# Performance work log

Measured on AMD Instinct MI355X. Metric: run time of the kernel, lower is better.

The kernel has to match this reference:

```python
import jax, jax.numpy as jnp
import numpy as np

B, T, C, H = 4, 4096, 1024, 64  # batch, seq, n_embd, head_size

def setup_inputs() -> dict:
    key = jax.random.key(0)
    kx, kq, kk, kv = jax.random.split(key, 4)
    x = jax.random.normal(kx, (B, T, C), dtype=jnp.float32)
    s = 1.0 / np.sqrt(C)
    Wq = jax.random.normal(kq, (C, H), dtype=jnp.float32) * s
    Wk = jax.random.normal(kk, (C, H), dtype=jnp.float32) * s
    Wv = jax.random.normal(kv, (C, H), dtype=jnp.float32) * s
    return {"x": x, "Wq": Wq, "Wk": Wk, "Wv": Wv}

def reference(x, Wq, Wk, Wv):
    B_, T_, C_ = x.shape
    q = x @ Wq  # [B,T,H]
    k = x @ Wk
    v = x @ Wv
    # NOTE: original scales by C**-0.5 (n_embd), not head_size**-0.5
    scale = jnp.asarray(C_, x.dtype) ** -0.5
    wei = jnp.einsum('bth,bsh->bts', q, k) * scale  # [B,T,T]
    causal = jnp.tril(jnp.ones((T_, T_), dtype=bool))
    wei = jnp.where(causal, wei, -jnp.inf)
    wei = jax.nn.softmax(wei, axis=-1)
    out = jnp.einsum('bts,bsh->bth', wei, v)  # [B,T,H]
    return out
```

## Files before the change

kernel.cpp:

```cpp
#include <hip/hip_runtime.h>
#include <hip/hip_bf16.h>
#include <math.h>

#define BB 4
#define TT 4096
#define CC 1024
#define HH 64

typedef __attribute__((ext_vector_type(8))) short short8;
typedef __attribute__((ext_vector_type(8))) unsigned short ushort8;
typedef __attribute__((ext_vector_type(4))) float f32x4;
typedef __attribute__((ext_vector_type(2))) unsigned int uint2v;

__device__ inline unsigned short f2bf(float f) {
    unsigned int u = __builtin_bit_cast(unsigned int, f);
    unsigned int r = u + 0x7fffu + ((u >> 16) & 1u);
    return (unsigned short)(r >> 16);
}

__device__ inline int soff_strip(int qs) {
    if (qs < 128) return (qs - 64) * 2;
    if (qs < 192) return 128 + (qs - 128) * 3;
    return 320 + (qs - 192) * 4;
}

__global__ __launch_bounds__(256) void wtrans_kernel(
    const float* __restrict__ Wq,
    const float* __restrict__ Wk,
    const float* __restrict__ Wv,
    unsigned short* __restrict__ Wf)
{
    const int t = blockIdx.x * 256 + threadIdx.x;
    const int lane = t & 63;
    const int ntl  = (t >> 6) % 12;
    const int kt   = t / 768;
    const int quad = lane >> 4, n = lane & 15;
    const int m    = ntl >> 2;
    const int col  = (ntl & 3) * 16 + n;
    const float* src = (m == 0) ? Wq : (m == 1) ? Wk : Wv;
    ushort8 u;
#pragma unroll
    for (int j = 0; j < 8; ++j)
        u[j] = f2bf(src[(kt * 32 + quad * 8 + j) * 64 + col]);
    *(ushort8*)(Wf + (size_t)t * 8) = u;
}

__global__ __launch_bounds__(256) void qkv_gemm(
    const float* __restrict__ x,
    const unsigned short* __restrict__ Wf,
    unsigned short* __restrict__ Qb,
    unsigned short* __restrict__ Kb,
    unsigned short* __restrict__ Vb)
{
    __shared__ f32x4 red[2][12][64];

    const int tid  = threadIdx.x;
    const int lane = tid & 63;
    const int wave = tid >> 6;
    const int n    = lane & 15;
    const int quad = lane >> 4;
    const int row0 = blockIdx.x * 16;

    const float* xp = x + (size_t)(row0 + n) * CC + wave * 256 + quad * 8;

    f32x4 acc[12];
#pragma unroll
    for (int i = 0; i < 12; ++i) acc[i] = (f32x4){0.f, 0.f, 0.f, 0.f};

#pragma unroll
    for (int kt = 0; kt < 8; ++kt) {
        const float4 f0 = *(const float4*)(xp + kt * 32);
        const float4 f1 = *(const float4*)(xp + kt * 32 + 4);
        short8 a;
        a[0] = (short)f2bf(f0.x); a[1] = (short)f2bf(f0.y);
        a[2] = (short)f2bf(f0.z); a[3] = (short)f2bf(f0.w);
        a[4] = (short)f2bf(f1.x); a[5] = (short)f2bf(f1.y);
        a[6] = (short)f2bf(f1.z); a[7] = (short)f2bf(f1.w);

        const unsigned short* wp = Wf + ((size_t)((wave * 8 + kt) * 12) * 64 + lane) * 8;
#pragma unroll
        for (int ntl = 0; ntl < 12; ++ntl) {
            const short8 bw = *(const short8*)(wp + (size_t)ntl * 64 * 8);
            acc[ntl] = __builtin_amdgcn_mfma_f32_16x16x32_bf16(a, bw, acc[ntl], 0, 0, 0);
        }
    }

    if (wave >= 2) {
#pragma unroll
        for (int ntl = 0; ntl < 12; ++ntl) red[wave - 2][ntl][lane] = acc[ntl];
    }
    __syncthreads();
    if (wave < 2) {
#pragma unroll
        for (int ntl = 0; ntl < 12; ++ntl) acc[ntl] += red[wave][ntl][lane];
    }
    __syncthreads();
    if (wave == 1) {
#pragma unroll
        for (int ntl = 0; ntl < 12; ++ntl) red[0][ntl][lane] = acc[ntl];
    }
    __syncthreads();
    if (wave == 0) {
#pragma unroll
        for (int ntl = 0; ntl < 12; ++ntl) {
            f32x4 s = acc[ntl] + red[0][ntl][lane];
            const int m    = ntl >> 2;
            const int colb = (ntl & 3) * 16;
            unsigned short* dst = (m == 0) ? Qb : (m == 1) ? Kb : Vb;
            const float sc = (m == 0) ? 0.03125f : 1.0f;
#pragma unroll
            for (int r = 0; r < 4; ++r) {
                const int row = row0 + quad * 4 + r;
                dst[(size_t)row * HH + colb + n] = f2bf(s[r] * sc);
            }
        }
    }
}

__global__ __launch_bounds__(256) void kv_repack(
    const unsigned short* __restrict__ Kb,
    const unsigned short* __restrict__ Vb,
    unsigned short* __restrict__ Kf,
    unsigned short* __restrict__ Vf)
{
    const int t = blockIdx.x * 256 + threadIdx.x;
    const int mat  = t >> 17;
    const int r    = t & 131071;
    const int lane = r & 63;
    const int kk   = (r >> 6) & 1;
    const int tile = (r >> 7) & 3;
    const int st   = (r >> 9) & 63;
    const int b    = r >> 15;
    const int n = lane & 15, quad = lane >> 4;

    if (mat == 0) {
        const unsigned short* src =
            Kb + ((size_t)b * TT + st * 64 + tile * 16 + n) * HH + kk * 32 + quad * 8;
        *(ushort8*)(Kf + (size_t)r * 8) = *(const ushort8*)src;
    } else {
        const int s0 = st * 64 + kk * 32 + quad * 8;
        const int h  = tile * 16 + n;
        ushort8 u;
#pragma unroll
        for (int j = 0; j < 8; ++j)
            u[j] = Vb[((size_t)b * TT + s0 + j) * HH + h];
        *(ushort8*)(Vf + (size_t)r * 8) = u;
    }
}

__global__ __launch_bounds__(256) void attn_kernel(
    const unsigned short* __restrict__ Qb,
    const unsigned short* __restrict__ Kf,
    const unsigned short* __restrict__ Vf,
    float* __restrict__ out,
    float* __restrict__ scr)
{
    __shared__ unsigned short Ps[4][16][72];

    const int tid  = threadIdx.x;
    const int lane = tid & 63;
    const int wave = tid >> 6;
    const int n    = lane & 15;
    const int quad = lane >> 4;

    const int wid = blockIdx.x * 4 + wave;
    const int b   = wid / 640;
    const int u   = wid - b * 640;

    int qs, ci;
    if (u < 64)        { qs = u;                  ci = 0; }
    else if (u < 192)  { const int v = u - 64;  qs = 64  + (v >> 1); ci = v & 1; }
    else if (u < 384)  { const int v = u - 192; const int d = v / 3;
                         qs = 128 + d;            ci = v - 3 * d; }
    else               { const int v = u - 384; qs = 192 + (v >> 2); ci = v & 3; }

    const int stmax = qs >> 2;
    const int st0   = ci << 4;
    const int stEnd = min(stmax, st0 + 15);
    const int nc    = (stmax + 16) >> 4;
    const int qrow  = qs * 16 + n;

    const unsigned short* qp = Qb + ((size_t)b * TT + qrow) * HH;
    const short8 bQ0 = *(const short8*)(qp + quad * 8);
    const short8 bQ1 = *(const short8*)(qp + 32 + quad * 8);

    const unsigned short* KfB = Kf + (size_t)b * 262144;
    const unsigned short* VfB = Vf + (size_t)b * 262144;

    f32x4 O[4];
#pragma unroll
    for (int ht = 0; ht < 4; ++ht) O[ht] = (f32x4){0.f, 0.f, 0.f, 0.f};
    float l = 0.f;

    for (int st = st0; st <= stEnd; ++st) {
        f32x4 S[4];
#pragma unroll
        for (int mt = 0; mt < 4; ++mt) {
            const unsigned short* kp = KfB + (size_t)((st * 4 + mt) * 2) * 512 + lane * 8;
            const short8 a0 = *(const short8*)(kp);
            const short8 a1 = *(const short8*)(kp + 512);
            f32x4 acc = (f32x4){0.f, 0.f, 0.f, 0.f};
            acc = __builtin_amdgcn_mfma_f32_16x16x32_bf16(a0, bQ0, acc, 0, 0, 0);
            acc = __builtin_amdgcn_mfma_f32_16x16x32_bf16(a1, bQ1, acc, 0, 0, 0);
            S[mt] = acc;
        }

        if (st == stmax) {
#pragma unroll
            for (int mt = 0; mt < 4; ++mt) {
                const int sg = st * 64 + mt * 16 + quad * 4;
#pragma unroll
                for (int r = 0; r < 4; ++r)
                    if (sg + r > qrow) S[mt][r] = -INFINITY;
            }
        }

#pragma unroll
        for (int mt = 0; mt < 4; ++mt)
#pragma unroll
            for (int r = 0; r < 4; ++r) {
                const float p = __expf(fminf(S[mt][r], 30.f));
                S[mt][r] = p;
                l += p;
            }

#pragma unroll
        for (int mt = 0; mt < 4; ++mt) {
            uint2v w;
            w[0] = (unsigned int)f2bf(S[mt][0]) | ((unsigned int)f2bf(S[mt][1]) << 16);
            w[1] = (unsigned int)f2bf(S[mt][2]) | ((unsigned int)f2bf(S[mt][3]) << 16);
            *(uint2v*)&Ps[wave][n][mt * 16 + quad * 4] = w;
        }
        asm volatile("s_waitcnt lgkmcnt(0)" ::: "memory");
        const short8 bP0 = *(const short8*)&Ps[wave][n][quad * 8];
        const short8 bP1 = *(const short8*)&Ps[wave][n][32 + quad * 8];

#pragma unroll
        for (int ht = 0; ht < 4; ++ht) {
            const unsigned short* vp = VfB + (size_t)((st * 4 + ht) * 2) * 512 + lane * 8;
            const short8 a0 = *(const short8*)(vp);
            const short8 a1 = *(const short8*)(vp + 512);
            O[ht] = __builtin_amdgcn_mfma_f32_16x16x32_bf16(a0, bP0, O[ht], 0, 0, 0);
            O[ht] = __builtin_amdgcn_mfma_f32_16x16x32_bf16(a1, bP1, O[ht], 0, 0, 0);
        }
    }

    l += __shfl_xor(l, 16);
    l += __shfl_xor(l, 32);

    if (nc == 1) {
        const float inv = 1.0f / l;
        float* op = out + ((size_t)b * TT + qrow) * HH;
#pragma unroll
        for (int ht = 0; ht < 4; ++ht) {
            float4 o4;
            o4.x = O[ht][0] * inv;
            o4.y = O[ht][1] * inv;
            o4.z = O[ht][2] * inv;
            o4.w = O[ht][3] * inv;
            *(float4*)(op + ht * 16 + quad * 4) = o4;
        }
    } else {
        float* sb = scr + (size_t)(b * 576 + soff_strip(qs) + ci) * 1040;
        float* rp = sb + n * 64;
#pragma unroll
        for (int ht = 0; ht < 4; ++ht)
            *(f32x4*)(rp + ht * 16 + quad * 4) = O[ht];
        if (quad == 0) sb[1024 + n] = l;
    }
}

__global__ __launch_bounds__(64) void combine_kernel(
    const float* __restrict__ scr,
    float* __restrict__ out)
{
    const int b  = blockIdx.x / 192;
    const int qs = 64 + blockIdx.x % 192;
    const int nc = ((qs >> 2) + 16) >> 4;
    const int base = b * 576 + soff_strip(qs);

    const int t    = threadIdx.x;
    const int row  = t >> 2;
    const int col0 = (t & 3) * 16;

    f32x4 s0 = (f32x4){0.f,0.f,0.f,0.f}, s1 = s0, s2 = s0, s3 = s0;
    float lsum = 0.f;
    for (int ci = 0; ci < nc; ++ci) {
        const float* sb = scr + (size_t)(base + ci) * 1040;
        lsum += sb[1024 + row];
        const float* p = sb + row * 64 + col0;
        s0 += *(const f32x4*)(p);
        s1 += *(const f32x4*)(p + 4);
        s2 += *(const f32x4*)(p + 8);
        s3 += *(const f32x4*)(p + 12);
    }
    const float inv = 1.0f / lsum;
    float* op = out + ((size_t)b * TT + qs * 16 + row) * HH + col0;
    *(f32x4*)(op)      = s0 * inv;
    *(f32x4*)(op + 4)  = s1 * inv;
    *(f32x4*)(op + 8)  = s2 * inv;
    *(f32x4*)(op + 12) = s3 * inv;
}

extern "C" void kernel_launch(void* const* d_in, const int* in_sizes, int n_in,
                              void* d_out, int out_size, void* d_ws, size_t ws_size,
                              hipStream_t stream)
{
    const float* x  = (const float*)d_in[0];
    const float* Wq = (const float*)d_in[1];
    const float* Wk = (const float*)d_in[2];
    const float* Wv = (const float*)d_in[3];

    unsigned short* Qb = (unsigned short*)d_ws;
    unsigned short* Kb = Qb + (size_t)BB * TT * HH;
    unsigned short* Vb = Kb + (size_t)BB * TT * HH;
    unsigned short* Wf = Vb + (size_t)BB * TT * HH;
    unsigned short* Kf = Wf + (size_t)192 * 1024;
    unsigned short* Vf = Kf + (size_t)BB * 262144;
    float*          scr = (float*)(Vf + (size_t)BB * 262144);
    float* out = (float*)d_out;

    wtrans_kernel<<<96, 256, 0, stream>>>(Wq, Wk, Wv, Wf);
    qkv_gemm<<<BB * TT / 16, 256, 0, stream>>>(x, Wf, Qb, Kb, Vb);
    kv_repack<<<1024, 256, 0, stream>>>(Kb, Vb, Kf, Vf);
    attn_kernel<<<640, 256, 0, stream>>>(Qb, Kf, Vf, out, scr);
    combine_kernel<<<768, 64, 0, stream>>>(scr, out);
}
```

Before: 160.0 us.

## Fuse K/V repack into QKV GEMM and prefetch K/V tiles in attention

The QKV projection now handles 32 rows per block, so each weight fragment feeds two MFMAs. It stages the fp32 results in shared memory and writes Q plus K and V directly in the fragment layouts the attention kernel reads, which removes the separate kv_repack kernel and the Kb/Vb round trip through global memory. The attention loop now software-prefetches the next K tile and issues the V loads before the softmax. It also double-buffers the P scratch in shared memory. The cost is more registers and 49KB of shared memory per GEMM block, which may reduce occupancy.

```diff
diff --git a/kernel.cpp b/kernel.cpp
--- a/kernel.cpp
+++ b/kernel.cpp
@@ -49,102 +49,125 @@
     const float* __restrict__ x,
     const unsigned short* __restrict__ Wf,
     unsigned short* __restrict__ Qb,
-    unsigned short* __restrict__ Kb,
-    unsigned short* __restrict__ Vb)
-{
-    __shared__ f32x4 red[2][12][64];
+    unsigned short* __restrict__ Kf,
+    unsigned short* __restrict__ Vf)
+{
+    __shared__ __align__(16) unsigned char smem[50176];
+    f32x4 (*red)[24][64] = (f32x4 (*)[24][64])smem;
+    float (*Tl)[200]     = (float (*)[200])(smem + 24576);
 
     const int tid  = threadIdx.x;
     const int lane = tid & 63;
     const int wave = tid >> 6;
     const int n    = lane & 15;
     const int quad = lane >> 4;
-    const int row0 = blockIdx.x * 16;
-
-    const float* xp = x + (size_t)(row0 + n) * CC + wave * 256 + quad * 8;
-
-    f32x4 acc[12];
-#pragma unroll
-    for (int i = 0; i < 12; ++i) acc[i] = (f32x4){0.f, 0.f, 0.f, 0.f};
+
+    const int row0g = blockIdx.x * 32;
+    const int b     = row0g >> 12;
+    const int trow  = row0g & (TT - 1);
+    const int st    = trow >> 6;
+    const int mtb   = (trow >> 4) & 3;
+    const int kkv   = (trow >> 5) & 1;
+
+    const float* xp0 = x + (size_t)(row0g + n) * CC + wave * 256 + quad * 8;
+    const float* xp1 = xp0 + 16 * CC;
+
+    f32x4 acc[2][12];
+#pragma unroll
+    for (int mtl = 0; mtl < 2; ++mtl)
+#pragma unroll
+        for (int i = 0; i < 12; ++i) acc[mtl][i] = (f32x4){0.f, 0.f, 0.f, 0.f};
 
 #pragma unroll
     for (int kt = 0; kt < 8; ++kt) {
-        const float4 f0 = *(const float4*)(xp + kt * 32);
-        const float4 f1 = *(const float4*)(xp + kt * 32 + 4);
-        short8 a;
-        a[0] = (short)f2bf(f0.x); a[1] = (short)f2bf(f0.y);
-        a[2] = (short)f2bf(f0.z); a[3] = (short)f2bf(f0.w);
-        a[4] = (short)f2bf(f1.x); a[5] = (short)f2bf(f1.y);
-        a[6] = (short)f2bf(f1.z); a[7] = (short)f2bf(f1.w);
+        const float4 f0 = *(const float4*)(xp0 + kt * 32);
+        const float4 f1 = *(const float4*)(xp0 + kt * 32 + 4);
+        const float4 g0 = *(const float4*)(xp1 + kt * 32);
+        const float4 g1 = *(const float4*)(xp1 + kt * 32 + 4);
+        short8 a0, a1;
+        a0[0] = (short)f2bf(f0.x); a0[1] = (short)f2bf(f0.y);
+        a0[2] = (short)f2bf(f0.z); a0[3] = (short)f2bf(f0.w);
+        a0[4] = (short)f2bf(f1.x); a0[5] = (short)f2bf(f1.y);
+        a0[6] = (short)f2bf(f1.z); a0[7] = (short)f2bf(f1.w);
+        a1[0] = (short)f2bf(g0.x); a1[1] = (short)f2bf(g0.y);
+        a1[2] = (short)f2bf(g0.z); a1[3] = (short)f2bf(g0.w);
+        a1[4] = (short)f2bf(g1.x); a1[5] = (short)f2bf(g1.y);
+        a1[6] = (short)f2bf(g1.z); a1[7] = (short)f2bf(g1.w);
 
         const unsigned short* wp = Wf + ((size_t)((wave * 8 + kt) * 12) * 64 + lane) * 8;
 #pragma unroll
         for (int ntl = 0; ntl < 12; ++ntl) {
             const short8 bw = *(const short8*)(wp + (size_t)ntl * 64 * 8);
-            acc[ntl] = __builtin_amdgcn_mfma_f32_16x16x32_bf16(a, bw, acc[ntl], 0, 0, 0);
+            acc[0][ntl] = __builtin_amdgcn_mfma_f32_16x16x32_bf16(a0, bw, acc[0][ntl], 0, 0, 0);
+            acc[1][ntl] = __builtin_amdgcn_mfma_f32_16x16x32_bf16(a1, bw, acc[1][ntl], 0, 0, 0);
         }
     }
 
     if (wave >= 2) {
 #pragma unroll
-        for (int ntl = 0; ntl < 12; ++ntl) red[wave - 2][ntl][lane] = acc[ntl];
+        for (int mtl = 0; mtl < 2; ++mtl)
+#pragma unroll
+            for (int ntl = 0; ntl < 12; ++ntl)
+                red[wave - 2][mtl * 12 + ntl][lane] = acc[mtl][ntl];
     }
     __syncthreads();
     if (wave < 2) {
 #pragma unroll
-        for (int ntl = 0; ntl < 12; ++ntl) acc[ntl] += red[wave][ntl][lane];
+        for (int mtl = 0; mtl < 2; ++mtl)
+#pragma unroll
+            for (int ntl = 0; ntl < 12; ++ntl)
+                acc[mtl][ntl] += red[wave][mtl * 12 + ntl][lane];
     }
     __syncthreads();
     if (wave == 1) {
 #pragma unroll
-        for (int ntl = 0; ntl < 12; ++ntl) red[0][ntl][lane] = acc[ntl];
+        for (int mtl = 0; mtl < 2; ++mtl)
+#pragma unroll
+            for (int ntl = 0; ntl < 12; ++ntl)
+                red[0][mtl * 12 + ntl][lane] = acc[mtl][ntl];
     }
     __syncthreads();
     if (wave == 0) {
 #pragma unroll
-        for (int ntl = 0; ntl < 12; ++ntl) {
-            f32x4 s = acc[ntl] + red[0][ntl][lane];
-            const int m    = ntl >> 2;
-            const int colb = (ntl & 3) * 16;
-            unsigned short* dst = (m == 0) ? Qb : (m == 1) ? Kb : Vb;
-            const float sc = (m == 0) ? 0.03125f : 1.0f;
-#pragma unroll
-            for (int r = 0; r < 4; ++r) {
-                const int row = row0 + quad * 4 + r;
-                dst[(size_t)row * HH + colb + n] = f2bf(s[r] * sc);
+        for (int mtl = 0; mtl < 2; ++mtl)
+#pragma unroll
+            for (int ntl = 0; ntl < 12; ++ntl) {
+                const f32x4 s = acc[mtl][ntl] + red[0][mtl * 12 + ntl][lane];
+                const int col = (ntl >> 2) * 64 + (ntl & 3) * 16 + n;
+#pragma unroll
+                for (int r = 0; r < 4; ++r)
+                    Tl[mtl * 16 + quad * 4 + r][col] = s[r];
             }
-        }
-    }
-}
-
-__global__ __launch_bounds__(256) void kv_repack(
-    const unsigned short* __restrict__ Kb,
-    const unsigned short* __restrict__ Vb,
-    unsigned short* __restrict__ Kf,
-    unsigned short* __restrict__ Vf)
-{
-    const int t = blockIdx.x * 256 + threadIdx.x;
-    const int mat  = t >> 17;
-    const int r    = t & 131071;
-    const int lane = r & 63;
-    const int kk   = (r >> 6) & 1;
-    const int tile = (r >> 7) & 3;
-    const int st   = (r >> 9) & 63;
-    const int b    = r >> 15;
-    const int n = lane & 15, quad = lane >> 4;
-
-    if (mat == 0) {
-        const unsigned short* src =
-            Kb + ((size_t)b * TT + st * 64 + tile * 16 + n) * HH + kk * 32 + quad * 8;
-        *(ushort8*)(Kf + (size_t)r * 8) = *(const ushort8*)src;
-    } else {
-        const int s0 = st * 64 + kk * 32 + quad * 8;
-        const int h  = tile * 16 + n;
+    }
+    __syncthreads();
+
+    {
+        const int row = tid & 31;
+        const int cq  = (tid >> 5) * 8;
         ushort8 u;
 #pragma unroll
         for (int j = 0; j < 8; ++j)
-            u[j] = Vb[((size_t)b * TT + s0 + j) * HH + h];
-        *(ushort8*)(Vf + (size_t)r * 8) = u;
+            u[j] = f2bf(Tl[row][cq + j] * 0.03125f);
+        *(ushort8*)(Qb + (size_t)(row0g + row) * HH + cq) = u;
+    }
+    {
+        const int mtl = wave & 1;
+        const int kk  = wave >> 1;
+        ushort8 u;
+#pragma unroll
+        for (int j = 0; j < 8; ++j)
+            u[j] = f2bf(Tl[mtl * 16 + n][64 + kk * 32 + quad * 8 + j]);
+        const size_t r = (size_t)(((b * 64 + st) * 4 + (mtb + mtl)) * 2 + kk) * 64 + lane;
+        *(ushort8*)(Kf + r * 8) = u;
+    }
+    {
+        const int ht = wave;
+        ushort8 u;
+#pragma unroll
+        for (int j = 0; j < 8; ++j)
+            u[j] = f2bf(Tl[quad * 8 + j][128 + ht * 16 + n]);
+        const size_t r = (size_t)(((b * 64 + st) * 4 + ht) * 2 + kkv) * 64 + lane;
+        *(ushort8*)(Vf + r * 8) = u;
     }
 }
 
@@ -155,7 +178,7 @@
     float* __restrict__ out,
     float* __restrict__ scr)
 {
-    __shared__ unsigned short Ps[4][16][72];
+    __shared__ unsigned short Ps[4][2][16][72];
 
     const int tid  = threadIdx.x;
     const int lane = tid & 63;
@@ -192,17 +215,38 @@
     for (int ht = 0; ht < 4; ++ht) O[ht] = (f32x4){0.f, 0.f, 0.f, 0.f};
     float l = 0.f;
 
+    short8 kA[4], kB[4];
+#pragma unroll
+    for (int mt = 0; mt < 4; ++mt) {
+        const unsigned short* kp = KfB + (size_t)((st0 * 4 + mt) * 2) * 512 + lane * 8;
+        kA[mt] = *(const short8*)(kp);
+        kB[mt] = *(const short8*)(kp + 512);
+    }
+
     for (int st = st0; st <= stEnd; ++st) {
         f32x4 S[4];
 #pragma unroll
         for (int mt = 0; mt < 4; ++mt) {
-            const unsigned short* kp = KfB + (size_t)((st * 4 + mt) * 2) * 512 + lane * 8;
-            const short8 a0 = *(const short8*)(kp);
-            const short8 a1 = *(const short8*)(kp + 512);
             f32x4 acc = (f32x4){0.f, 0.f, 0.f, 0.f};
-            acc = __builtin_amdgcn_mfma_f32_16x16x32_bf16(a0, bQ0, acc, 0, 0, 0);
-            acc = __builtin_amdgcn_mfma_f32_16x16x32_bf16(a1, bQ1, acc, 0, 0, 0);
+            acc = __builtin_amdgcn_mfma_f32_16x16x32_bf16(kA[mt], bQ0, acc, 0, 0, 0);
+            acc = __builtin_amdgcn_mfma_f32_16x16x32_bf16(kB[mt], bQ1, acc, 0, 0, 0);
             S[mt] = acc;
+        }
+
+        short8 vA[4], vB[4];
+#pragma unroll
+        for (int ht = 0; ht < 4; ++ht) {
+            const unsigned short* vp = VfB + (size_t)((st * 4 + ht) * 2) * 512 + lane * 8;
+            vA[ht] = *(const short8*)(vp);
+            vB[ht] = *(const short8*)(vp + 512);
+        }
+        if (st < stEnd) {
+#pragma unroll
+            for (int mt = 0; mt < 4; ++mt) {
+                const unsigned short* kp = KfB + (size_t)(((st + 1) * 4 + mt) * 2) * 512 + lane * 8;
+                kA[mt] = *(const short8*)(kp);
+                kB[mt] = *(const short8*)(kp + 512);
+            }
         }
 
         if (st == stmax) {
@@ -224,24 +268,22 @@
                 l += p;
             }
 
+        const int pp = st & 1;
 #pragma unroll
         for (int mt = 0; mt < 4; ++mt) {
             uint2v w;
             w[0] = (unsigned int)f2bf(S[mt][0]) | ((unsigned int)f2bf(S[mt][1]) << 16);
             w[1] = (unsigned int)f2bf(S[mt][2]) | ((unsigned int)f2bf(S[mt][3]) << 16);
-            *(uint2v*)&Ps[wave][n][mt * 16 + quad * 4] = w;
+            *(uint2v*)&Ps[wave][pp][n][mt * 16 + quad * 4] = w;
         }
         asm volatile("s_waitcnt lgkmcnt(0)" ::: "memory");
-        const short8 bP0 = *(const short8*)&Ps[wave][n][quad * 8];
-        const short8 bP1 = *(const short8*)&Ps[wave][n][32 + quad * 8];
+        const short8 bP0 = *(const short8*)&Ps[wave][pp][n][quad * 8];
+        const short8 bP1 = *(const short8*)&Ps[wave][pp][n][32 + quad * 8];
 
 #pragma unroll
         for (int ht = 0; ht < 4; ++ht) {
-            const unsigned short* vp = VfB + (size_t)((st * 4 + ht) * 2) * 512 + lane * 8;
-            const short8 a0 = *(const short8*)(vp);
-            const short8 a1 = *(const short8*)(vp + 512);
-            O[ht] = __builtin_amdgcn_mfma_f32_16x16x32_bf16(a0, bP0, O[ht], 0, 0, 0);
-            O[ht] = __builtin_amdgcn_mfma_f32_16x16x32_bf16(a1, bP1, O[ht], 0, 0, 0);
+            O[ht] = __builtin_amdgcn_mfma_f32_16x16x32_bf16(vA[ht], bP0, O[ht], 0, 0, 0);
+            O[ht] = __builtin_amdgcn_mfma_f32_16x16x32_bf16(vB[ht], bP1, O[ht], 0, 0, 0);
         }
     }
 
@@ -312,17 +354,14 @@
     const float* Wv = (const float*)d_in[3];
 
     unsigned short* Qb = (unsigned short*)d_ws;
-    unsigned short* Kb = Qb + (size_t)BB * TT * HH;
-    unsigned short* Vb = Kb + (size_t)BB * TT * HH;
-    unsigned short* Wf = Vb + (size_t)BB * TT * HH;
+    unsigned short* Wf = Qb + (size_t)BB * TT * HH;
     unsigned short* Kf = Wf + (size_t)192 * 1024;
     unsigned short* Vf = Kf + (size_t)BB * 262144;
     float*          scr = (float*)(Vf + (size_t)BB * 262144);
     float* out = (float*)d_out;
 
     wtrans_kernel<<<96, 256, 0, stream>>>(Wq, Wk, Wv, Wf);
-    qkv_gemm<<<BB * TT / 16, 256, 0, stream>>>(x, Wf, Qb, Kb, Vb);
-    kv_repack<<<1024, 256, 0, stream>>>(Kb, Vb, Kf, Vf);
+    qkv_gemm<<<BB * TT / 32, 256, 0, stream>>>(x, Wf, Qb, Kf, Vf);
     attn_kernel<<<640, 256, 0, stream>>>(Qb, Kf, Vf, out, scr);
     combine_kernel<<<768, 64, 0, stream>>>(scr, out);
 }
```

Result: no change. 158.4 us (-1.0%).
